# Performance work log

Measured on AMD Instinct MI355X. Metric: run time of the kernel, lower is better.

Reference implementation:

```python
import jax, jax.numpy as jnp
import numpy as np

SEQ, B, IN, H, L = 256, 512, 300, 512, 256
EPS = 1e-5


def setup_inputs() -> dict:
    key = jax.random.key(0)
    ks = jax.random.split(key, 10)
    s_ih = 1.0 / np.sqrt(H)
    return {
        "x": jax.random.normal(ks[0], (SEQ, B, IN), dtype=jnp.float32),
        "W_ih": jax.random.normal(ks[1], (4 * H, IN), dtype=jnp.float32) * s_ih,
        "W_hh": jax.random.normal(ks[2], (4 * H, H), dtype=jnp.float32) * s_ih,
        "b_ih": jax.random.normal(ks[3], (4 * H,), dtype=jnp.float32) * s_ih,
        "b_hh": jax.random.normal(ks[4], (4 * H,), dtype=jnp.float32) * s_ih,
        "bn1_gamma": jnp.ones((H,), dtype=jnp.float32),
        "bn1_beta": jnp.zeros((H,), dtype=jnp.float32),
        "W1": jax.random.normal(ks[5], (L, H), dtype=jnp.float32) / np.sqrt(H),
        "b1": jax.random.normal(ks[6], (L,), dtype=jnp.float32) * 0.01,
        "bn2_gamma": jnp.ones((L,), dtype=jnp.float32),
        "bn2_beta": jnp.zeros((L,), dtype=jnp.float32),
        "W2": jax.random.normal(ks[7], (1, L), dtype=jnp.float32) / np.sqrt(L),
        "b2": jax.random.normal(ks[8], (1,), dtype=jnp.float32) * 0.01,
    }


def _batchnorm(x, gamma, beta):
    # training-mode BatchNorm1d: batch statistics, biased variance
    mean = jnp.mean(x, axis=0)
    var = jnp.var(x, axis=0)
    return (x - mean) * jax.lax.rsqrt(var + EPS) * gamma + beta


def reference(x, W_ih, W_hh, b_ih, b_hh, bn1_gamma, bn1_beta, W1, b1,
              bn2_gamma, bn2_beta, W2, b2):
    # Pre-compute the input projection for all timesteps in one big GEMM:
    # [S, B, IN] @ [IN, 4H] -> [S, B, 4H]
    x_proj = jnp.einsum('sbi,gi->sbg', x, W_ih) + b_ih + b_hh

    def step(carry, xt):
        h, c = carry
        gates = xt + h @ W_hh.T  # [B, 4H]
        i, f, g, o = jnp.split(gates, 4, axis=-1)
        i = jax.nn.sigmoid(i)
        f = jax.nn.sigmoid(f)
        g = jnp.tanh(g)
        o = jax.nn.sigmoid(o)
        c = f * c + i * g
        h = o * jnp.tanh(c)
        return (h, c), None

    h0 = jnp.zeros((x.shape[1], H), dtype=x.dtype)
    c0 = jnp.zeros((x.shape[1], H), dtype=x.dtype)
    (h, _c), _ = jax.lax.scan(step, (h0, c0), x_proj)
    # dropout with training=False -> identity

    h = _batchnorm(h, bn1_gamma, bn1_beta)
    h = h @ W1.T + b1
    h = _batchnorm(h, bn2_gamma, bn2_beta)
    h = jax.nn.relu(h)
    out = h @ W2.T + b2            # [B, 1]
    out = 4.0 * jax.nn.sigmoid(out)
    return out.squeeze(-1)         # [B]
```

## Files before the change

### kernel.cpp

```cpp
#include <hip/hip_runtime.h>
#include <math.h>

constexpr int SEQ   = 256;
constexpr int BATCH = 512;
constexpr int INDIM = 300;
constexpr int KIH   = 320;
constexpr int HDIM  = 512;
constexpr int LDIM  = 256;
constexpr int G4    = 4 * HDIM;

typedef _Float16 f16x8 __attribute__((ext_vector_type(8)));
typedef _Float16 f16x4 __attribute__((ext_vector_type(4)));
typedef float    f32x4 __attribute__((ext_vector_type(4)));


__global__ __launch_bounds__(256) void prep_weights_kernel(
    const float* __restrict__ Wih, const float* __restrict__ Whh,
    const float* __restrict__ bih, const float* __restrict__ bhh,
    _Float16* __restrict__ slab, float* __restrict__ bsum)
{
    const int by = blockIdx.x >> 6;
    const int rl = blockIdx.x & 63;
    const int g  = rl >> 4, r = rl & 15;
    const int grow = g * HDIM + by * 16 + r;
    const int tid = threadIdx.x;
    if (tid < 208) {
        const int col0 = tid * 4;
        f16x4 v;
        #pragma unroll
        for (int e = 0; e < 4; ++e) {
            const int col = col0 + e;
            float f;
            if (col < KIH) f = (col < INDIM) ? Wih[(size_t)grow * INDIM + col] : 0.f;
            else           f = Whh[(size_t)grow * HDIM + (col - KIH)];
            v[e] = (_Float16)f;
        }
        *(f16x4*)(slab + ((size_t)(by * 64 + rl)) * 832 + col0) = v;
    } else if (tid == 208) {
        bsum[grow] = bih[grow] + bhh[grow];
    }
}

__global__ __launch_bounds__(256) void prep_x_kernel(
    const float* __restrict__ x, _Float16* __restrict__ xall)
{
    const int rowl = threadIdx.x >> 6;
    const int s    = threadIdx.x & 63;
    const int row  = blockIdx.x * 4 + rowl;
    if (s >= 40) return;
    const int k0 = s * 8;
    const float* xr = x + (size_t)row * INDIM;
    f16x8 v;
    #pragma unroll
    for (int e = 0; e < 8; ++e)
        v[e] = (k0 + e < INDIM) ? (_Float16)xr[k0 + e] : (_Float16)0.f;
    *(f16x8*)(xall + (size_t)row * KIH + k0) = v;
}

__global__ __launch_bounds__(512, 2) void lstm_persist8(
    const _Float16* __restrict__ xall,
    const _Float16* __restrict__ slab,
    _Float16* __restrict__ hb,
    float* __restrict__ h32,
    const float* __restrict__ bsum,
    int* __restrict__ cnt)
{
    __shared__ _Float16 act[5][64][72];
    __shared__ float    Gb[64][68];

    const int tid  = threadIdx.x;
    const int wid  = tid >> 6;
    const int lane = tid & 63;
    const int gh   = wid >> 1;
    const int bh   = wid & 1;
    const int l15  = lane & 15;
    const int q4   = lane >> 4;
    const int bx   = blockIdx.x & 7;
    const int by   = blockIdx.x >> 3;
    const int b0   = bx * 64;
    const int hc0  = by * 16;

    f16x8 wreg[13][2];
    {
        const _Float16* sb = slab + (size_t)by * 64 * 832
                                  + (size_t)(gh * 16 + l15) * 832 + q4 * 8;
        #pragma unroll
        for (int ch = 0; ch < 13; ++ch)
            #pragma unroll
            for (int kl = 0; kl < 2; ++kl)
                wreg[ch][kl] = *(const f16x8*)(sb + ch * 64 + kl * 32);
    }

    const int srow = tid >> 3;
    const int suu  = tid & 7;

    const int bl  = tid >> 3;
    const int j0l = (tid & 7) * 2;
    const int bg  = b0 + bl;
    const int jg  = hc0 + j0l;
    float bsv[4][2];
    #pragma unroll
    for (int g = 0; g < 4; ++g) {
        bsv[g][0] = bsum[g * HDIM + jg];
        bsv[g][1] = bsum[g * HDIM + jg + 1];
    }
    float cv0 = 0.f, cv1 = 0.f;

#define BARX() do { asm volatile("" ::: "memory");                           \
                    __builtin_amdgcn_s_barrier();                            \
                    asm volatile("" ::: "memory"); } while (0)
#define LGKM0() asm volatile("s_waitcnt lgkmcnt(0)" ::: "memory")
#define VM0()   asm volatile("s_waitcnt vmcnt(0)" ::: "memory")

#define LH(J, DST) do {                                                      \
    const unsigned long long* _p = (const unsigned long long*)               \
        (hbase + (size_t)srow * HDIM + (J) * 64 + suu * 8);                  \
    union { unsigned long long u[2]; f16x8 v; } _t;                          \
    _t.u[0] = __hip_atomic_load(_p,     __ATOMIC_RELAXED,                    \
                                __HIP_MEMORY_SCOPE_AGENT);                  \
    _t.u[1] = __hip_atomic_load(_p + 1, __ATOMIC_RELAXED,                    \
                                __HIP_MEMORY_SCOPE_AGENT);                  \
    DST = _t.v; } while (0)

#define CCH(SLOT, CH) do {                                                   \
    _Pragma("unroll")                                                        \
    for (int kl = 0; kl < 2; ++kl) {                                         \
        const f16x8 bf0 = *(const f16x8*)&act[SLOT][bh*32 +      l15][kl*32 + q4*8]; \
        const f16x8 bf1 = *(const f16x8*)&act[SLOT][bh*32 + 16 + l15][kl*32 + q4*8]; \
        acc0 = __builtin_amdgcn_mfma_f32_16x16x32_f16(wreg[CH][kl], bf0, acc0, 0, 0, 0); \
        acc1 = __builtin_amdgcn_mfma_f32_16x16x32_f16(wreg[CH][kl], bf1, acc1, 0, 0, 0); \
    } } while (0)

    for (int t = 0; t < SEQ; ++t) {
        const _Float16* xbase = xall + ((size_t)t * BATCH + b0) * KIH;
        const _Float16* hbase = hb + (size_t)(t & 1) * BATCH * HDIM
                                   + (size_t)b0 * HDIM;
        f32x4 acc0 = {0.f,0.f,0.f,0.f}, acc1 = {0.f,0.f,0.f,0.f};
        f16x8 xr[5], hr[5], hr2[3];

        #pragma unroll
        for (int ch = 0; ch < 5; ++ch)
            xr[ch] = *(const f16x8*)(xbase + (size_t)srow * KIH + ch * 64 + suu * 8);
        if (t > 0) {
            const int* fp = cnt + bx * 32 + (lane & 31);
            int wd = 0;
            for (;;) {
                const int f = __hip_atomic_load(fp, __ATOMIC_RELAXED,
                                                __HIP_MEMORY_SCOPE_AGENT);
                if (__all(f >= t)) break;
                if (++wd > (1 << 20)) break;
                __builtin_amdgcn_s_sleep(1);
            }
        }
        LH(0, hr[0]); LH(1, hr[1]); LH(2, hr[2]); LH(3, hr[3]); LH(4, hr[4]);
        #pragma unroll
        for (int ch = 0; ch < 5; ++ch)
            *(f16x8*)&act[ch][srow][suu * 8] = xr[ch];
        LGKM0(); BARX();

        CCH(0, 0); CCH(1, 1); CCH(2, 2); CCH(3, 3); CCH(4, 4);
        BARX();

        #pragma unroll
        for (int j = 0; j < 5; ++j)
            *(f16x8*)&act[j][srow][suu * 8] = hr[j];
        LH(5, hr2[0]); LH(6, hr2[1]); LH(7, hr2[2]);
        LGKM0(); BARX();

        CCH(0, 5); CCH(1, 6); CCH(2, 7); CCH(3, 8); CCH(4, 9);
        BARX();

        #pragma unroll
        for (int j = 0; j < 3; ++j)
            *(f16x8*)&act[j][srow][suu * 8] = hr2[j];
        LGKM0(); BARX();

        CCH(0, 10); CCH(1, 11); CCH(2, 12);
        {
            #pragma unroll
            for (int q = 0; q < 4; ++q) {
                Gb[gh * 16 + q4 * 4 + q][bh * 32 +      l15] = acc0[q];
                Gb[gh * 16 + q4 * 4 + q][bh * 32 + 16 + l15] = acc1[q];
            }
        }
        LGKM0(); BARX();

        {
            float hv0, hv1;
            {
                float vi = Gb[0 * 16 + j0l][bl] + bsv[0][0];
                float vf = Gb[1 * 16 + j0l][bl] + bsv[1][0];
                float vg = Gb[2 * 16 + j0l][bl] + bsv[2][0];
                float vo = Gb[3 * 16 + j0l][bl] + bsv[3][0];
                vi = 1.f / (1.f + __expf(-vi));
                vf = 1.f / (1.f + __expf(-vf));
                vg = 1.f - 2.f / (__expf(2.f * vg) + 1.f);
                vo = 1.f / (1.f + __expf(-vo));
                const float cc = vf * cv0 + vi * vg;
                cv0 = cc;
                hv0 = vo * (1.f - 2.f / (__expf(2.f * cc) + 1.f));
            }
            {
                float vi = Gb[0 * 16 + j0l + 1][bl] + bsv[0][1];
                float vf = Gb[1 * 16 + j0l + 1][bl] + bsv[1][1];
                float vg = Gb[2 * 16 + j0l + 1][bl] + bsv[2][1];
                float vo = Gb[3 * 16 + j0l + 1][bl] + bsv[3][1];
                vi = 1.f / (1.f + __expf(-vi));
                vf = 1.f / (1.f + __expf(-vf));
                vg = 1.f - 2.f / (__expf(2.f * vg) + 1.f);
                vo = 1.f / (1.f + __expf(-vo));
                const float cc = vf * cv1 + vi * vg;
                cv1 = cc;
                hv1 = vo * (1.f - 2.f / (__expf(2.f * cc) + 1.f));
            }
            union { unsigned int u; _Float16 v[2]; } hu;
            hu.v[0] = (_Float16)hv0; hu.v[1] = (_Float16)hv1;
            _Float16* hbw = hb + (size_t)((t + 1) & 1) * BATCH * HDIM;
            __hip_atomic_store((unsigned int*)(hbw + (size_t)bg * HDIM + jg),
                               hu.u, __ATOMIC_RELAXED, __HIP_MEMORY_SCOPE_AGENT);
            if (t == SEQ - 1) {
                float* hp = h32 + (size_t)bg * HDIM + jg;
                hp[0] = hv0; hp[1] = hv1;
            }
        }
        VM0(); BARX();
        if (tid == 0)
            __hip_atomic_store(&cnt[bx * 32 + by], t + 1, __ATOMIC_RELAXED,
                               __HIP_MEMORY_SCOPE_AGENT);
    }
#undef BARX
#undef LGKM0
#undef VM0
#undef LH
#undef CCH
}

__global__ __launch_bounds__(256) void prep_kernel(
    const float* __restrict__ Wih, const float* __restrict__ Whh,
    const float* __restrict__ bih, const float* __restrict__ bhh,
    _Float16* __restrict__ Wihc, _Float16* __restrict__ Whhc,
    float* __restrict__ bsum)
{
    const int g = blockIdx.x;
    for (int col = threadIdx.x; col < KIH; col += 256)
        Wihc[(size_t)g * KIH + col] =
            (col < INDIM) ? (_Float16)Wih[(size_t)g * INDIM + col] : (_Float16)0.f;
    for (int col = threadIdx.x; col < HDIM; col += 256)
        Whhc[(size_t)g * HDIM + col] = (_Float16)Whh[(size_t)g * HDIM + col];
    if (threadIdx.x == 0) bsum[g] = bih[g] + bhh[g];
}

__global__ __launch_bounds__(256) void fused_step_kernel(
    const float* __restrict__ xt, const _Float16* __restrict__ Wihc,
    const _Float16* __restrict__ Whhc, const float* __restrict__ bsum,
    float* __restrict__ c, float* __restrict__ h)
{
    __shared__ _Float16 As[32][72];
    __shared__ _Float16 Bs[128][72];
    __shared__ float    Gb[4][32][36];

    const int tid = threadIdx.x;
    const int b0  = blockIdx.x * 32;
    const int hc0 = blockIdx.y * 32;
    const int wid  = tid >> 6;
    const int lane = tid & 63;

    f32x4 acc[2][2] = {};
    const int arow = tid >> 3;
    const int ac8  = (tid & 7) * 8;
    const int brr  = tid >> 1;
    const int bseg = (tid & 1) * 32;

    for (int phase = 0; phase < 2; ++phase) {
        const float* Asrc = phase ? h : xt;
        const _Float16* Bsrc = phase ? Whhc : Wihc;
        const int Kpad = phase ? HDIM : KIH;
        const int Kval = phase ? HDIM : INDIM;
        const int astr = phase ? HDIM : INDIM;

        for (int k0 = 0; k0 < Kpad; k0 += 64) {
            const int gk = k0 + ac8;
            const float* pa = Asrc + (size_t)(b0 + arow) * astr + gk;
            float4 u = {0.f,0.f,0.f,0.f}, v = {0.f,0.f,0.f,0.f};
            if (gk + 3 < Kval)  u = *(const float4*)pa;
            if (gk + 7 < Kval)  v = *(const float4*)(pa + 4);
            f16x8 a8;
            a8[0]=(_Float16)u.x; a8[1]=(_Float16)u.y; a8[2]=(_Float16)u.z; a8[3]=(_Float16)u.w;
            a8[4]=(_Float16)v.x; a8[5]=(_Float16)v.y; a8[6]=(_Float16)v.z; a8[7]=(_Float16)v.w;
            const int grow = (brr >> 5) * HDIM + hc0 + (brr & 31);
            const _Float16* pb = Bsrc + (size_t)grow * Kpad + k0 + bseg;
            f16x8 w0 = *(const f16x8*)(pb + 0);
            f16x8 w1 = *(const f16x8*)(pb + 8);
            f16x8 w2 = *(const f16x8*)(pb + 16);
            f16x8 w3 = *(const f16x8*)(pb + 24);
            __syncthreads();
            *(f16x8*)&As[arow][ac8] = a8;
            *(f16x8*)&Bs[brr][bseg + 0]  = w0;
            *(f16x8*)&Bs[brr][bseg + 8]  = w1;
            *(f16x8*)&Bs[brr][bseg + 16] = w2;
            *(f16x8*)&Bs[brr][bseg + 24] = w3;
            __syncthreads();
            const int lr = lane & 15;
            const int lk = (lane >> 4) * 8;
            #pragma unroll
            for (int kf = 0; kf < 2; ++kf) {
                const int kl = kf * 32 + lk;
                f16x8 a0 = *(const f16x8*)&As[lr][kl];
                f16x8 a1 = *(const f16x8*)&As[16 + lr][kl];
                f16x8 bb0 = *(const f16x8*)&Bs[wid * 32 + lr][kl];
                f16x8 bb1 = *(const f16x8*)&Bs[wid * 32 + 16 + lr][kl];
                acc[0][0] = __builtin_amdgcn_mfma_f32_16x16x32_f16(a0, bb0, acc[0][0], 0, 0, 0);
                acc[0][1] = __builtin_amdgcn_mfma_f32_16x16x32_f16(a0, bb1, acc[0][1], 0, 0, 0);
                acc[1][0] = __builtin_amdgcn_mfma_f32_16x16x32_f16(a1, bb0, acc[1][0], 0, 0, 0);
                acc[1][1] = __builtin_amdgcn_mfma_f32_16x16x32_f16(a1, bb1, acc[1][1], 0, 0, 0);
            }
        }
    }
    __syncthreads();
    {
        const int cn = lane & 15;
        const int rbq = (lane >> 4) * 4;
        #pragma unroll
        for (int mi = 0; mi < 2; ++mi)
            #pragma unroll
            for (int ni = 0; ni < 2; ++ni)
                #pragma unroll
                for (int r = 0; r < 4; ++r)
                    Gb[wid][mi * 16 + rbq + r][ni * 16 + cn] = acc[mi][ni][r];
    }
    __syncthreads();
    {
        const int bl  = tid >> 3;
        const int jl0 = (tid & 7) * 4;
        const int gb  = b0 + bl;
        const int gj  = hc0 + jl0;
        const f32x4 ig = *(const f32x4*)&Gb[0][bl][jl0];
        const f32x4 fg = *(const f32x4*)&Gb[1][bl][jl0];
        const f32x4 gg = *(const f32x4*)&Gb[2][bl][jl0];
        const f32x4 og = *(const f32x4*)&Gb[3][bl][jl0];
        const f32x4 bi = *(const f32x4*)&bsum[0 * HDIM + gj];
        const f32x4 bf = *(const f32x4*)&bsum[1 * HDIM + gj];
        const f32x4 bg = *(const f32x4*)&bsum[2 * HDIM + gj];
        const f32x4 bo = *(const f32x4*)&bsum[3 * HDIM + gj];
        float* cp = c + (size_t)gb * HDIM + gj;
        float* hp = h + (size_t)gb * HDIM + gj;
        f32x4 cvv = *(const f32x4*)cp;
        f32x4 hv;
        #pragma unroll
        for (int q = 0; q < 4; ++q) {
            const float iv = 1.f / (1.f + __expf(-(ig[q] + bi[q])));
            const float fv = 1.f / (1.f + __expf(-(fg[q] + bf[q])));
            const float gv = tanhf(gg[q] + bg[q]);
            const float ov = 1.f / (1.f + __expf(-(og[q] + bo[q])));
            const float cc = fv * cvv[q] + iv * gv;
            cvv[q] = cc;
            hv[q] = ov * tanhf(cc);
        }
        *(f32x4*)cp = cvv;
        *(f32x4*)hp = hv;
    }
}

__global__ __launch_bounds__(256) void bn_stats_kernel(
    const float* __restrict__ X, int nfeat,
    const float* __restrict__ gamma, const float* __restrict__ beta,
    float* __restrict__ s, float* __restrict__ t)
{
    const int f = blockIdx.x * 256 + threadIdx.x;
    if (f >= nfeat) return;
    float sum = 0.f, sq = 0.f;
    for (int b = 0; b < BATCH; ++b) {
        const float v = X[(size_t)b * nfeat + f];
        sum += v; sq += v * v;
    }
    const float mean = sum * (1.f / BATCH);
    const float var  = sq * (1.f / BATCH) - mean * mean;
    const float rstd = rsqrtf(var + 1e-5f);
    const float sc   = gamma[f] * rstd;
    s[f] = sc;
    t[f] = beta[f] - mean * sc;
}

__global__ __launch_bounds__(256) void fc1_kernel(
    const float* __restrict__ h, const float* __restrict__ s1,
    const float* __restrict__ t1, const float* __restrict__ W1,
    const float* __restrict__ b1, float* __restrict__ out1)
{
    const int b = blockIdx.x;
    const int l = threadIdx.x;
    const float* hbp = h  + (size_t)b * HDIM;
    const float* wl  = W1 + (size_t)l * HDIM;
    float acc = 0.f;
    for (int k = 0; k < HDIM; ++k)
        acc += (hbp[k] * s1[k] + t1[k]) * wl[k];
    out1[(size_t)b * LDIM + l] = acc + b1[l];
}

__global__ __launch_bounds__(256) void final_kernel(
    const float* __restrict__ out1, const float* __restrict__ s2,
    const float* __restrict__ t2, const float* __restrict__ W2,
    const float* __restrict__ b2, float* __restrict__ out)
{
    const int b = blockIdx.x;
    float v = out1[(size_t)b * LDIM + threadIdx.x];
    v = v * s2[threadIdx.x] + t2[threadIdx.x];
    v = fmaxf(v, 0.f);
    v *= W2[threadIdx.x];
    #pragma unroll
    for (int off = 32; off > 0; off >>= 1) v += __shfl_down(v, off);
    __shared__ float red[4];
    if ((threadIdx.x & 63) == 0) red[threadIdx.x >> 6] = v;
    __syncthreads();
    if (threadIdx.x == 0) {
        const float ssum = red[0] + red[1] + red[2] + red[3] + b2[0];
        out[b] = 4.f / (1.f + expf(-ssum));
    }
}

extern "C" void kernel_launch(void* const* d_in, const int* in_sizes, int n_in,
                              void* d_out, int out_size, void* d_ws, size_t ws_size,
                              hipStream_t stream) {
    const float* x   = (const float*)d_in[0];
    const float* Wih = (const float*)d_in[1];
    const float* Whh = (const float*)d_in[2];
    const float* bih = (const float*)d_in[3];
    const float* bhh = (const float*)d_in[4];
    const float* g1  = (const float*)d_in[5];
    const float* be1 = (const float*)d_in[6];
    const float* W1  = (const float*)d_in[7];
    const float* b1  = (const float*)d_in[8];
    const float* g2  = (const float*)d_in[9];
    const float* be2 = (const float*)d_in[10];
    const float* W2  = (const float*)d_in[11];
    const float* b2  = (const float*)d_in[12];
    float* out = (float*)d_out;

    const size_t SZ_XALL = (size_t)(SEQ + 1) * BATCH * KIH * 2;
    const size_t SZ_SLAB = (size_t)32 * 64 * 832 * 2;
    const size_t SZ_HB   = (size_t)2 * BATCH * HDIM * 2;
    const size_t SZ_H32  = (size_t)BATCH * HDIM * 4;
    const size_t SZ_BSUM = (size_t)G4 * 4;
    const size_t SZ_CNT  = (size_t)SEQ * 8 * 4;
    const size_t SZ_ST   = (size_t)(HDIM * 2 + LDIM * 2) * 4;
    const size_t SZ_OUT1 = (size_t)BATCH * LDIM * 4;
    const size_t NEED = SZ_XALL + SZ_SLAB + SZ_HB + SZ_H32 + SZ_BSUM +
                        SZ_CNT + SZ_ST + SZ_OUT1;

    if (ws_size >= NEED) {
        char* p = (char*)d_ws;
        _Float16* xall = (_Float16*)p;           p += SZ_XALL;
        _Float16* slab = (_Float16*)p;           p += SZ_SLAB;
        _Float16* hbuf = (_Float16*)p;           p += SZ_HB;
        float* h32     = (float*)p;              p += SZ_H32;
        float* bsum    = (float*)p;              p += SZ_BSUM;
        int*   cnt     = (int*)p;                p += SZ_CNT;
        float* s1 = (float*)p;                   p += HDIM * 4;
        float* t1 = (float*)p;                   p += HDIM * 4;
        float* s2 = (float*)p;                   p += LDIM * 4;
        float* t2 = (float*)p;                   p += LDIM * 4;
        float* out1 = (float*)p;

        hipMemsetAsync(hbuf, 0, SZ_HB, stream);
        hipMemsetAsync(cnt, 0, SZ_CNT, stream);
        prep_weights_kernel<<<2048, 256, 0, stream>>>(Wih, Whh, bih, bhh, slab, bsum);
        prep_x_kernel<<<SEQ * 128, 256, 0, stream>>>(x, xall);

        lstm_persist8<<<dim3(256), dim3(512), 0, stream>>>(
            xall, slab, hbuf, h32, bsum, cnt);

        bn_stats_kernel<<<2, 256, 0, stream>>>(h32, HDIM, g1, be1, s1, t1);
        fc1_kernel<<<BATCH, 256, 0, stream>>>(h32, s1, t1, W1, b1, out1);
        bn_stats_kernel<<<1, 256, 0, stream>>>(out1, LDIM, g2, be2, s2, t2);
        final_kernel<<<BATCH, 256, 0, stream>>>(out1, s2, t2, W2, b2, out);
    } else {
        float* ws   = (float*)d_ws;
        float* h    = ws;
        float* c    = h + BATCH * HDIM;
        float* bsum = c + BATCH * HDIM;
        float* s1   = bsum + G4;
        float* t1   = s1 + HDIM;
        float* s2   = t1 + HDIM;
        float* t2   = s2 + LDIM;
        float* out1 = t2 + LDIM;
        _Float16* Wihc = (_Float16*)(out1 + (size_t)BATCH * LDIM);
        _Float16* Whhc = Wihc + (size_t)G4 * KIH;

        hipMemsetAsync(h, 0, (size_t)2 * BATCH * HDIM * sizeof(float), stream);
        prep_kernel<<<G4, 256, 0, stream>>>(Wih, Whh, bih, bhh, Wihc, Whhc, bsum);
        const dim3 sgrid(BATCH / 32, HDIM / 32);
        for (int t = 0; t < SEQ; ++t) {
            fused_step_kernel<<<sgrid, 256, 0, stream>>>(
                x + (size_t)t * BATCH * INDIM, Wihc, Whhc, bsum, c, h);
        }
        bn_stats_kernel<<<2, 256, 0, stream>>>(h, HDIM, g1, be1, s1, t1);
        fc1_kernel<<<BATCH, 256, 0, stream>>>(h, s1, t1, W1, b1, out1);
        bn_stats_kernel<<<1, 256, 0, stream>>>(out1, LDIM, g2, be2, s2, t2);
        final_kernel<<<BATCH, 256, 0, stream>>>(out1, s2, t2, W2, b2, out);
    }
}
```

Before: 1.481 ms.

## Load MFMA operands directly from global memory and split K across waves

Reorganizes the persistent LSTM kernel's per-step GEMM. The x and h operands are no longer staged through shared memory. Each wave now loads its B fragments straight from global memory into registers and computes a 32x32 output tile over half of the K dimension. The two K-halves are reduced through a double shared buffer, which removes four of the six block barriers per timestep. In exchange, each wave holds more registers and issues more global loads, and the memory access pattern may be less coalesced.

Result: slower. 2.911 ms (+96.6%).

```diff
diff --git a/kernel.cpp b/kernel.cpp
--- a/kernel.cpp
+++ b/kernel.cpp
@@ -57,7 +57,7 @@
     *(f16x8*)(xall + (size_t)row * KIH + k0) = v;
 }
 
-__global__ __launch_bounds__(512, 2) void lstm_persist8(
+__global__ __launch_bounds__(512, 2) void lstm_persist9(
     const _Float16* __restrict__ xall,
     const _Float16* __restrict__ slab,
     _Float16* __restrict__ hb,
@@ -65,14 +65,14 @@
     const float* __restrict__ bsum,
     int* __restrict__ cnt)
 {
-    __shared__ _Float16 act[5][64][72];
-    __shared__ float    Gb[64][68];
+    __shared__ float Gb2[2][64][68];
 
     const int tid  = threadIdx.x;
     const int wid  = tid >> 6;
     const int lane = tid & 63;
-    const int gh   = wid >> 1;
-    const int bh   = wid & 1;
+    const int gg   = wid >> 2;
+    const int nt32 = (wid >> 1) & 1;
+    const int ks   = wid & 1;
     const int l15  = lane & 15;
     const int q4   = lane >> 4;
     const int bx   = blockIdx.x & 7;
@@ -80,19 +80,19 @@
     const int b0   = bx * 64;
     const int hc0  = by * 16;
 
-    f16x8 wreg[13][2];
+    f16x8 ws[13][2];
     {
         const _Float16* sb = slab + (size_t)by * 64 * 832
-                                  + (size_t)(gh * 16 + l15) * 832 + q4 * 8;
-        #pragma unroll
-        for (int ch = 0; ch < 13; ++ch)
-            #pragma unroll
-            for (int kl = 0; kl < 2; ++kl)
-                wreg[ch][kl] = *(const f16x8*)(sb + ch * 64 + kl * 32);
-    }
-
-    const int srow = tid >> 3;
-    const int suu  = tid & 7;
+                                  + (size_t)(gg * 32 + l15) * 832 + ks * 32 + q4 * 8;
+        #pragma unroll
+        for (int ch = 0; ch < 13; ++ch) {
+            ws[ch][0] = *(const f16x8*)(sb + ch * 64);
+            ws[ch][1] = *(const f16x8*)(sb + 16 * 832 + ch * 64);
+        }
+    }
+
+    const size_t xoff = (size_t)(b0 + nt32 * 32 + l15) * KIH  + ks * 32 + q4 * 8;
+    const size_t hoff = (size_t)(b0 + nt32 * 32 + l15) * HDIM + ks * 32 + q4 * 8;
 
     const int bl  = tid >> 3;
     const int j0l = (tid & 7) * 2;
@@ -112,35 +112,36 @@
 #define LGKM0() asm volatile("s_waitcnt lgkmcnt(0)" ::: "memory")
 #define VM0()   asm volatile("s_waitcnt vmcnt(0)" ::: "memory")
 
-#define LH(J, DST) do {                                                      \
-    const unsigned long long* _p = (const unsigned long long*)               \
-        (hbase + (size_t)srow * HDIM + (J) * 64 + suu * 8);                  \
-    union { unsigned long long u[2]; f16x8 v; } _t;                          \
-    _t.u[0] = __hip_atomic_load(_p,     __ATOMIC_RELAXED,                    \
+#define LHPAIR(J, D0, D1) do {                                               \
+    const unsigned long long* _p0 = (const unsigned long long*)              \
+        (hbv + (J) * 64);                                                    \
+    const unsigned long long* _p1 = (const unsigned long long*)              \
+        (hbv + 16 * HDIM + (J) * 64);                                        \
+    union { unsigned long long u[2]; f16x8 v; } _a, _b;                      \
+    _a.u[0] = __hip_atomic_load(_p0,     __ATOMIC_RELAXED,                   \
                                 __HIP_MEMORY_SCOPE_AGENT);                  \
-    _t.u[1] = __hip_atomic_load(_p + 1, __ATOMIC_RELAXED,                    \
+    _a.u[1] = __hip_atomic_load(_p0 + 1, __ATOMIC_RELAXED,                   \
                                 __HIP_MEMORY_SCOPE_AGENT);                  \
-    DST = _t.v; } while (0)
-
-#define CCH(SLOT, CH) do {                                                   \
-    _Pragma("unroll")                                                        \
-    for (int kl = 0; kl < 2; ++kl) {                                         \
-        const f16x8 bf0 = *(const f16x8*)&act[SLOT][bh*32 +      l15][kl*32 + q4*8]; \
-        const f16x8 bf1 = *(const f16x8*)&act[SLOT][bh*32 + 16 + l15][kl*32 + q4*8]; \
-        acc0 = __builtin_amdgcn_mfma_f32_16x16x32_f16(wreg[CH][kl], bf0, acc0, 0, 0, 0); \
-        acc1 = __builtin_amdgcn_mfma_f32_16x16x32_f16(wreg[CH][kl], bf1, acc1, 0, 0, 0); \
-    } } while (0)
+    _b.u[0] = __hip_atomic_load(_p1,     __ATOMIC_RELAXED,                   \
+                                __HIP_MEMORY_SCOPE_AGENT);                  \
+    _b.u[1] = __hip_atomic_load(_p1 + 1, __ATOMIC_RELAXED,                   \
+                                __HIP_MEMORY_SCOPE_AGENT);                  \
+    D0 = _a.v; D1 = _b.v; } while (0)
 
     for (int t = 0; t < SEQ; ++t) {
-        const _Float16* xbase = xall + ((size_t)t * BATCH + b0) * KIH;
-        const _Float16* hbase = hb + (size_t)(t & 1) * BATCH * HDIM
-                                   + (size_t)b0 * HDIM;
-        f32x4 acc0 = {0.f,0.f,0.f,0.f}, acc1 = {0.f,0.f,0.f,0.f};
-        f16x8 xr[5], hr[5], hr2[3];
-
-        #pragma unroll
-        for (int ch = 0; ch < 5; ++ch)
-            xr[ch] = *(const f16x8*)(xbase + (size_t)srow * KIH + ch * 64 + suu * 8);
+        const _Float16* xbv = xall + (size_t)t * BATCH * KIH + xoff;
+        const _Float16* hbv = hb + (size_t)(t & 1) * BATCH * HDIM + hoff;
+
+        f32x4 acc00 = {0.f,0.f,0.f,0.f}, acc01 = {0.f,0.f,0.f,0.f};
+        f32x4 acc10 = {0.f,0.f,0.f,0.f}, acc11 = {0.f,0.f,0.f,0.f};
+
+        f16x8 bx0[5], bx1[5];
+        #pragma unroll
+        for (int ch = 0; ch < 5; ++ch) {
+            bx0[ch] = *(const f16x8*)(xbv + ch * 64);
+            bx1[ch] = *(const f16x8*)(xbv + 16 * KIH + ch * 64);
+        }
+
         if (t > 0) {
             const int* fp = cnt + bx * 32 + (lane & 31);
             int wd = 0;
@@ -151,64 +152,65 @@
                 if (++wd > (1 << 20)) break;
                 __builtin_amdgcn_s_sleep(1);
             }
-        }
-        LH(0, hr[0]); LH(1, hr[1]); LH(2, hr[2]); LH(3, hr[3]); LH(4, hr[4]);
-        #pragma unroll
-        for (int ch = 0; ch < 5; ++ch)
-            *(f16x8*)&act[ch][srow][suu * 8] = xr[ch];
+            asm volatile("" ::: "memory");
+        }
+
+        f16x8 bh0[8], bh1[8];
+        #pragma unroll
+        for (int j = 0; j < 4; ++j) LHPAIR(j, bh0[j], bh1[j]);
+
+        #pragma unroll
+        for (int ch = 0; ch < 5; ++ch) {
+            acc00 = __builtin_amdgcn_mfma_f32_16x16x32_f16(ws[ch][0], bx0[ch], acc00, 0, 0, 0);
+            acc01 = __builtin_amdgcn_mfma_f32_16x16x32_f16(ws[ch][0], bx1[ch], acc01, 0, 0, 0);
+            acc10 = __builtin_amdgcn_mfma_f32_16x16x32_f16(ws[ch][1], bx0[ch], acc10, 0, 0, 0);
+            acc11 = __builtin_amdgcn_mfma_f32_16x16x32_f16(ws[ch][1], bx1[ch], acc11, 0, 0, 0);
+        }
+
+        #pragma unroll
+        for (int j = 4; j < 8; ++j) LHPAIR(j, bh0[j], bh1[j]);
+
+        #pragma unroll
+        for (int j = 0; j < 8; ++j) {
+            acc00 = __builtin_amdgcn_mfma_f32_16x16x32_f16(ws[5+j][0], bh0[j], acc00, 0, 0, 0);
+            acc01 = __builtin_amdgcn_mfma_f32_16x16x32_f16(ws[5+j][0], bh1[j], acc01, 0, 0, 0);
+            acc10 = __builtin_amdgcn_mfma_f32_16x16x32_f16(ws[5+j][1], bh0[j], acc10, 0, 0, 0);
+            acc11 = __builtin_amdgcn_mfma_f32_16x16x32_f16(ws[5+j][1], bh1[j], acc11, 0, 0, 0);
+        }
+
+        #pragma unroll
+        for (int q = 0; q < 4; ++q) {
+            Gb2[ks][gg * 32 +      q4 * 4 + q][nt32 * 32 +      l15] = acc00[q];
+            Gb2[ks][gg * 32 +      q4 * 4 + q][nt32 * 32 + 16 + l15] = acc01[q];
+            Gb2[ks][gg * 32 + 16 + q4 * 4 + q][nt32 * 32 +      l15] = acc10[q];
+            Gb2[ks][gg * 32 + 16 + q4 * 4 + q][nt32 * 32 + 16 + l15] = acc11[q];
+        }
         LGKM0(); BARX();
 
-        CCH(0, 0); CCH(1, 1); CCH(2, 2); CCH(3, 3); CCH(4, 4);
-        BARX();
-
-        #pragma unroll
-        for (int j = 0; j < 5; ++j)
-            *(f16x8*)&act[j][srow][suu * 8] = hr[j];
-        LH(5, hr2[0]); LH(6, hr2[1]); LH(7, hr2[2]);
-        LGKM0(); BARX();
-
-        CCH(0, 5); CCH(1, 6); CCH(2, 7); CCH(3, 8); CCH(4, 9);
-        BARX();
-
-        #pragma unroll
-        for (int j = 0; j < 3; ++j)
-            *(f16x8*)&act[j][srow][suu * 8] = hr2[j];
-        LGKM0(); BARX();
-
-        CCH(0, 10); CCH(1, 11); CCH(2, 12);
         {
+            float pre[4][2];
             #pragma unroll
-            for (int q = 0; q < 4; ++q) {
-                Gb[gh * 16 + q4 * 4 + q][bh * 32 +      l15] = acc0[q];
-                Gb[gh * 16 + q4 * 4 + q][bh * 32 + 16 + l15] = acc1[q];
+            for (int g = 0; g < 4; ++g) {
+                pre[g][0] = Gb2[0][g * 16 + j0l    ][bl]
+                          + Gb2[1][g * 16 + j0l    ][bl] + bsv[g][0];
+                pre[g][1] = Gb2[0][g * 16 + j0l + 1][bl]
+                          + Gb2[1][g * 16 + j0l + 1][bl] + bsv[g][1];
             }
-        }
-        LGKM0(); BARX();
-
-        {
             float hv0, hv1;
             {
-                float vi = Gb[0 * 16 + j0l][bl] + bsv[0][0];
-                float vf = Gb[1 * 16 + j0l][bl] + bsv[1][0];
-                float vg = Gb[2 * 16 + j0l][bl] + bsv[2][0];
-                float vo = Gb[3 * 16 + j0l][bl] + bsv[3][0];
-                vi = 1.f / (1.f + __expf(-vi));
-                vf = 1.f / (1.f + __expf(-vf));
-                vg = 1.f - 2.f / (__expf(2.f * vg) + 1.f);
-                vo = 1.f / (1.f + __expf(-vo));
+                float vi = 1.f / (1.f + __expf(-pre[0][0]));
+                float vf = 1.f / (1.f + __expf(-pre[1][0]));
+                float vg = 1.f - 2.f / (__expf(2.f * pre[2][0]) + 1.f);
+                float vo = 1.f / (1.f + __expf(-pre[3][0]));
                 const float cc = vf * cv0 + vi * vg;
                 cv0 = cc;
                 hv0 = vo * (1.f - 2.f / (__expf(2.f * cc) + 1.f));
             }
             {
-                float vi = Gb[0 * 16 + j0l + 1][bl] + bsv[0][1];
-                float vf = Gb[1 * 16 + j0l + 1][bl] + bsv[1][1];
-                float vg = Gb[2 * 16 + j0l + 1][bl] + bsv[2][1];
-                float vo = Gb[3 * 16 + j0l + 1][bl] + bsv[3][1];
-                vi = 1.f / (1.f + __expf(-vi));
-                vf = 1.f / (1.f + __expf(-vf));
-                vg = 1.f - 2.f / (__expf(2.f * vg) + 1.f);
-                vo = 1.f / (1.f + __expf(-vo));
+                float vi = 1.f / (1.f + __expf(-pre[0][1]));
+                float vf = 1.f / (1.f + __expf(-pre[1][1]));
+                float vg = 1.f - 2.f / (__expf(2.f * pre[2][1]) + 1.f);
+                float vo = 1.f / (1.f + __expf(-pre[3][1]));
                 const float cc = vf * cv1 + vi * vg;
                 cv1 = cc;
                 hv1 = vo * (1.f - 2.f / (__expf(2.f * cc) + 1.f));
@@ -231,8 +233,7 @@
 #undef BARX
 #undef LGKM0
 #undef VM0
-#undef LH
-#undef CCH
+#undef LHPAIR
 }
 
 __global__ __launch_bounds__(256) void prep_kernel(
@@ -465,7 +466,7 @@
         prep_weights_kernel<<<2048, 256, 0, stream>>>(Wih, Whh, bih, bhh, slab, bsum);
         prep_x_kernel<<<SEQ * 128, 256, 0, stream>>>(x, xall);
 
-        lstm_persist8<<<dim3(256), dim3(512), 0, stream>>>(
+        lstm_persist9<<<dim3(256), dim3(512), 0, stream>>>(
             xall, slab, hbuf, h32, bsum, cnt);
 
         bn_stats_kernel<<<2, 256, 0, stream>>>(h32, HDIM, g1, be1, s1, t1);
```
